# Optimization experiments

Measured on AMD Instinct MI355X. Metric: run time of the kernel, lower is better.

## Reference

```python
import jax, jax.numpy as jnp
import numpy as np

N_NODES = 100000
IN_DIM = 64
OUT_DIM = 64
N_EDGES = 1600000


def setup_inputs() -> dict:
    key = jax.random.key(0)
    k1, k2, k3, k4 = jax.random.split(key, 4)
    x = jax.random.normal(k1, (N_NODES, IN_DIM), dtype=jnp.float32)
    edge_index = jax.random.randint(k2, (2, N_EDGES), 0, N_NODES, dtype=jnp.int32)
    # nn.Linear(in_dim, out_dim): weight [out_dim, in_dim], bias [out_dim]
    bound = 1.0 / np.sqrt(IN_DIM)
    W = jax.random.uniform(k3, (OUT_DIM, IN_DIM), minval=-bound, maxval=bound, dtype=jnp.float32)
    b = jax.random.uniform(k4, (OUT_DIM,), minval=-bound, maxval=bound, dtype=jnp.float32)
    return {"x": x, "edge_index": edge_index, "W": W, "b": b}


def reference(x, edge_index, W, b):
    row, col = edge_index[0], edge_index[1]
    # gather neighbor features and scatter-add into destination rows: [N, in_dim]
    aggr = jax.ops.segment_sum(x[col], row, num_segments=x.shape[0])
    # linear + relu
    return jax.nn.relu(aggr @ W.T + b)
```

## Files before the change

kernel.cpp:

```cpp
#include <hip/hip_runtime.h>
#include <hip/hip_bf16.h>

#define DIM 64
#define BROWS 32
#define BSHIFT 5
#define REGCAP 2048
#define MAXB 4096
#define LCSR_CAP 1024
#define PCHUNK 8192

typedef __attribute__((ext_vector_type(8))) short bf16x8;
typedef __attribute__((ext_vector_type(4))) float f32x4;
typedef __attribute__((ext_vector_type(8))) ushort u16x8;

static __device__ __forceinline__ ushort f2bu(float f) {
  __hip_bfloat16 h = __float2bfloat16(f);
  return *reinterpret_cast<const ushort*>(&h);
}
static __device__ __forceinline__ float bu2f(ushort u) {
  return __uint_as_float(((unsigned)u) << 16);
}

__global__ __launch_bounds__(256) void zero_kernel(int* __restrict__ p, int n) {
  int i = blockIdx.x * 256 + threadIdx.x;
  if (i < n) p[i] = 0;
}

__global__ __launch_bounds__(512) void prep_part_kernel(
    const float* __restrict__ x, const float* __restrict__ W,
    const int* __restrict__ ei, ushort* __restrict__ xb,
    ushort* __restrict__ Wbf, int* __restrict__ bcur, uint* __restrict__ outU,
    int nNodes, int nEdges, int nB, int nPB) {
  __shared__ int h[MAXB];
  __shared__ int base[MAXB];
  const int t = threadIdx.x;

  const int idx = blockIdx.x * 512 + t;
  const int nx8 = nNodes * DIM / 8;
  if (idx < nx8) {
    const f32x4* p = (const f32x4*)(x + (size_t)idx * 8);
    f32x4 v0 = p[0], v1 = p[1];
    u16x8 o;
    o[0] = f2bu(v0[0]); o[1] = f2bu(v0[1]); o[2] = f2bu(v0[2]); o[3] = f2bu(v0[3]);
    o[4] = f2bu(v1[0]); o[5] = f2bu(v1[1]); o[6] = f2bu(v1[2]); o[7] = f2bu(v1[3]);
    *(u16x8*)(xb + (size_t)idx * 8) = o;
  }
  if (blockIdx.x == 0) {
    const int wb = t * 8;
    u16x8 o;
#pragma unroll
    for (int k = 0; k < 8; ++k) o[k] = f2bu(W[wb + k]);
    *(u16x8*)(Wbf + wb) = o;
    if (t < 8) {
      u16x8 z = {0, 0, 0, 0, 0, 0, 0, 0};
      *(u16x8*)(xb + (size_t)nNodes * DIM + t * 8) = z;
    }
  }

  if (blockIdx.x >= nPB) return;

  for (int i = t; i < nB; i += 512) h[i] = 0;
  __syncthreads();
  const int i0 = blockIdx.x * PCHUNK + t * 16;
  int4 r0, r1, r2, r3;
  const bool full = (i0 + 16 <= nEdges);
  if (full) {
    r0 = *(const int4*)(ei + i0);
    r1 = *(const int4*)(ei + i0 + 4);
    r2 = *(const int4*)(ei + i0 + 8);
    r3 = *(const int4*)(ei + i0 + 12);
#define CNT(R) atomicAdd(&h[(R) >> BSHIFT], 1);
    CNT(r0.x) CNT(r0.y) CNT(r0.z) CNT(r0.w)
    CNT(r1.x) CNT(r1.y) CNT(r1.z) CNT(r1.w)
    CNT(r2.x) CNT(r2.y) CNT(r2.z) CNT(r2.w)
    CNT(r3.x) CNT(r3.y) CNT(r3.z) CNT(r3.w)
#undef CNT
  } else if (i0 < nEdges) {
    for (int k = i0; k < nEdges; ++k) atomicAdd(&h[ei[k] >> BSHIFT], 1);
  }
  __syncthreads();
  for (int i = t; i < nB; i += 512) {
    int c = h[i];
    base[i] = c ? atomicAdd(&bcur[i], c) : 0;
  }
  __syncthreads();
  for (int i = t; i < nB; i += 512) h[i] = 0;
  __syncthreads();
#define PUT(RR, CC)                                                       \
  {                                                                       \
    int b_ = (RR) >> BSHIFT;                                              \
    int pos_ = base[b_] + atomicAdd(&h[b_], 1);                           \
    if (pos_ < REGCAP)                                                    \
      outU[(size_t)b_ * REGCAP + pos_] =                                  \
          (((uint)((RR) & (BROWS - 1))) << 27) | (((uint)(CC)) << 7);     \
  }
  if (full) {
    int4 c0 = *(const int4*)(ei + nEdges + i0);
    int4 c1 = *(const int4*)(ei + nEdges + i0 + 4);
    int4 c2 = *(const int4*)(ei + nEdges + i0 + 8);
    int4 c3 = *(const int4*)(ei + nEdges + i0 + 12);
    PUT(r0.x, c0.x) PUT(r0.y, c0.y) PUT(r0.z, c0.z) PUT(r0.w, c0.w)
    PUT(r1.x, c1.x) PUT(r1.y, c1.y) PUT(r1.z, c1.z) PUT(r1.w, c1.w)
    PUT(r2.x, c2.x) PUT(r2.y, c2.y) PUT(r2.z, c2.z) PUT(r2.w, c2.w)
    PUT(r3.x, c3.x) PUT(r3.y, c3.y) PUT(r3.z, c3.z) PUT(r3.w, c3.w)
  } else if (i0 < nEdges) {
    for (int k = i0; k < nEdges; ++k) {
      int row = ei[k], col = ei[nEdges + k];
      PUT(row, col)
    }
  }
#undef PUT
}

__global__ __launch_bounds__(256, 8) void bucket_gather_gemm_kernel(
    const char* __restrict__ xc, float* __restrict__ out,
    const int* __restrict__ bcur, const ushort* __restrict__ Wbf,
    const float* __restrict__ bias, int nNodes) {
  __shared__ int lcsr[LCSR_CAP];
  __shared__ int lhist[BROWS];
  __shared__ int loff[BROWS + 1];
  __shared__ int lcur[BROWS];
  __shared__ ushort sA[BROWS * DIM];

  const int t = threadIdx.x;
  const int bkt = blockIdx.x;
  const int w = t >> 6, lane = t & 63;
  const uint* streamU = (const uint*)(out + (size_t)bkt * REGCAP);
  int cnt = bcur[bkt];
  if (cnt > REGCAP) cnt = REGCAP;

  const bool fast = (cnt + BROWS * 8 <= LCSR_CAP);
  const int rbase = w * 8;

  if (t < BROWS) lhist[t] = 0;
  __syncthreads();

  if (fast) {
    uint p0 = 0, p1 = 0, p2 = 0;
    int nheld = 0;
    {
      int i = t;
      if (i < cnt) { p0 = streamU[i]; nheld = 1; i += 256; }
      if (i < cnt) { p1 = streamU[i]; nheld = 2; i += 256; }
      if (i < cnt) { p2 = streamU[i]; nheld = 3; }
    }
    if (nheld > 0) atomicAdd(&lhist[p0 >> 27], 1);
    if (nheld > 1) atomicAdd(&lhist[p1 >> 27], 1);
    if (nheld > 2) atomicAdd(&lhist[p2 >> 27], 1);
    __syncthreads();
    if (t < BROWS) {
      int d = lhist[t];
      int pd = (d + 7) & ~7;
      if (pd == 0) pd = 8;
      int v = pd;
#pragma unroll
      for (int o = 1; o < BROWS; o <<= 1) {
        int u = __shfl_up(v, o);
        if (t >= o) v += u;
      }
      loff[t] = v - pd;
      lcur[t] = v - pd;
      if (t == BROWS - 1) loff[BROWS] = v;
    }
    __syncthreads();
    if (nheld > 0) { int pos = atomicAdd(&lcur[p0 >> 27], 1); lcsr[pos] = (int)(p0 & 0x07ffffffu); }
    if (nheld > 1) { int pos = atomicAdd(&lcur[p1 >> 27], 1); lcsr[pos] = (int)(p1 & 0x07ffffffu); }
    if (nheld > 2) { int pos = atomicAdd(&lcur[p2 >> 27], 1); lcsr[pos] = (int)(p2 & 0x07ffffffu); }
    __syncthreads();
    if (t < BROWS) {
      int d = lhist[t];
      int pd = (d + 7) & ~7;
      if (pd == 0) pd = 8;
      int o0 = loff[t];
      for (int k = d; k < pd; ++k) lcsr[o0 + k] = nNodes << 7;
    }
    __syncthreads();

    const int half = lane >> 5;
    const int m = lane & 31;
    const char* xlp = xc + (m << 2);

#define ISSUE(v, E)                                   \
    {                                                 \
      int c0_ = lcsr[(E) + 0 + half];                 \
      int c1_ = lcsr[(E) + 2 + half];                 \
      int c2_ = lcsr[(E) + 4 + half];                 \
      int c3_ = lcsr[(E) + 6 + half];                 \
      v##0 = *(const uint*)(xlp + c0_);               \
      v##1 = *(const uint*)(xlp + c1_);               \
      v##2 = *(const uint*)(xlp + c2_);               \
      v##3 = *(const uint*)(xlp + c3_);               \
    }
#define CONSUME(v)                                                          \
    {                                                                       \
      float l01 = __uint_as_float(v##0 << 16) + __uint_as_float(v##1 << 16);\
      float l23 = __uint_as_float(v##2 << 16) + __uint_as_float(v##3 << 16);\
      aLo += l01 + l23;                                                     \
      float h01 = __uint_as_float(v##0 & 0xffff0000u) +                     \
                  __uint_as_float(v##1 & 0xffff0000u);                      \
      float h23 = __uint_as_float(v##2 & 0xffff0000u) +                     \
                  __uint_as_float(v##3 & 0xffff0000u);                      \
      aHi += h01 + h23;                                                     \
    }
#define BOUND                                                               \
    if (e + 8 == rEnd) {                                                    \
      float t0 = aLo + __shfl_xor(aLo, 32);                                 \
      float t1 = aHi + __shfl_xor(aHi, 32);                                 \
      if (lane < 32) {                                                      \
        uint pk = (((uint)f2bu(t1)) << 16) | (uint)f2bu(t0);                \
        int cs = (m >> 2) ^ (r & 7);                                        \
        ((uint*)sA)[r * 32 + cs * 4 + (m & 3)] = pk;                        \
      }                                                                     \
      aLo = 0.f; aHi = 0.f;                                                 \
      ++r;                                                                  \
      rEnd = (r < rbase + 8) ? loff[r + 1] : 0x7fffffff;                    \
    }

    int r = rbase;
    int rEnd = loff[r + 1];
    const int eBeg = loff[rbase];
    const int eEndW = loff[rbase + 8];
    float aLo = 0.f, aHi = 0.f;
    uint vA0, vA1, vA2, vA3, vB0, vB1, vB2, vB3, vC0, vC1, vC2, vC3;

    int e = eBeg;
    ISSUE(vA, e)
    ISSUE(vB, e + 8)
    ISSUE(vC, e + 16)
    for (;;) {
      CONSUME(vA)
      if (e + 24 < eEndW) ISSUE(vA, e + 24)
      BOUND
      e += 8; if (e >= eEndW) break;
      CONSUME(vB)
      if (e + 24 < eEndW) ISSUE(vB, e + 24)
      BOUND
      e += 8; if (e >= eEndW) break;
      CONSUME(vC)
      if (e + 24 < eEndW) ISSUE(vC, e + 24)
      BOUND
      e += 8; if (e >= eEndW) break;
    }
#undef ISSUE
#undef CONSUME
#undef BOUND
  } else {
    for (int rr = 0; rr < 8; ++rr) {
      int r = rbase + rr;
      float acc = 0.f;
      for (int i = 0; i < cnt; ++i) {
        uint p = streamU[i];
        if ((int)(p >> 27) == r)
          acc += bu2f(*(const ushort*)(xc + (p & 0x07ffffffu) + 2 * lane));
      }
      int cs = (lane >> 3) ^ (r & 7);
      sA[r * DIM + cs * 8 + (lane & 7)] = f2bu(acc);
    }
  }

  __syncthreads();

  const int rq = lane & 15, kg = lane >> 4;
  const int h16 = (w & 1) * 16;
  const int ch = w >> 1;
  const int row = h16 + rq;
  const ushort* pr = &sA[row * DIM];
  bf16x8 A0 = *(const bf16x8*)(pr + (((kg) ^ (row & 7)) << 3));
  bf16x8 A1 = *(const bf16x8*)(pr + (((4 + kg) ^ (row & 7)) << 3));

  f32x4 acc4[2] = {f32x4{0, 0, 0, 0}, f32x4{0, 0, 0, 0}};
#pragma unroll
  for (int jt = 0; jt < 2; ++jt) {
    const ushort* bRow = Wbf + (ch * 32 + jt * 16 + rq) * DIM + kg * 8;
    bf16x8 B0 = *(const bf16x8*)(bRow);
    bf16x8 B1 = *(const bf16x8*)(bRow + 32);
    acc4[jt] = __builtin_amdgcn_mfma_f32_16x16x32_bf16(A0, B0, acc4[jt], 0, 0, 0);
    acc4[jt] = __builtin_amdgcn_mfma_f32_16x16x32_bf16(A1, B1, acc4[jt], 0, 0, 0);
  }

  const int nodeBase = bkt * BROWS + h16;
#pragma unroll
  for (int jt = 0; jt < 2; ++jt) {
    int j = ch * 32 + jt * 16 + rq;
    float bj = bias[j];
#pragma unroll
    for (int q = 0; q < 4; ++q) {
      int node = nodeBase + kg * 4 + q;
      out[(size_t)node * DIM + j] = fmaxf(acc4[jt][q] + bj, 0.f);
    }
  }
}

__global__ __launch_bounds__(256) void scatter_add_kernel(
    const float* __restrict__ x, const int* __restrict__ ei,
    float* __restrict__ aggr, int nEdges) {
  const int lane = threadIdx.x & 63;
  const int e = blockIdx.x * 4 + (threadIdx.x >> 6);
  if (e >= nEdges) return;
  const int row = ei[e];
  const int col = ei[nEdges + e];
  atomicAdd(&aggr[(size_t)row * DIM + lane], x[(size_t)col * DIM + lane]);
}

__global__ __launch_bounds__(256) void linear_relu_inplace_kernel(
    float* __restrict__ io, const float* __restrict__ W,
    const float* __restrict__ b, int nRows) {
  __shared__ float sW[64][65];
  __shared__ float sRow[4][64];
  const int tid = threadIdx.x;
  for (int i = tid; i < 64 * 64; i += 256) sW[i >> 6][i & 63] = W[i];
  __syncthreads();
  const int wid = tid >> 6, j = tid & 63;
  const int row = blockIdx.x * 4 + wid;
  if (row < nRows) {
    const size_t base = (size_t)row * DIM;
    sRow[wid][j] = io[base + j];
    float acc = b[j];
#pragma unroll
    for (int k = 0; k < 64; ++k) acc = fmaf(sRow[wid][k], sW[j][k], acc);
    io[base + j] = fmaxf(acc, 0.0f);
  }
}

extern "C" void kernel_launch(void* const* d_in, const int* in_sizes, int n_in,
                              void* d_out, int out_size, void* d_ws, size_t ws_size,
                              hipStream_t stream) {
  const float* x = (const float*)d_in[0];
  const int* ei  = (const int*)d_in[1];
  const float* W = (const float*)d_in[2];
  const float* b = (const float*)d_in[3];
  float* out     = (float*)d_out;

  const int nNodes = in_sizes[0] / DIM;
  const int nEdges = in_sizes[1] / 2;
  const int nB = (nNodes + BROWS - 1) >> BSHIFT;

  size_t off = 0;
  auto take = [&](size_t bytes) {
    size_t r = off;
    off += (bytes + 255) & ~(size_t)255;
    return r;
  };
  char* ws = (char*)d_ws;
  int* bcur   = (int*)(ws + take(MAXB * 4));
  ushort* Wbf = (ushort*)(ws + take(DIM * DIM * 2));
  ushort* xb  = (ushort*)(ws + take((size_t)(nNodes + 1) * DIM * 2));

  const bool fastPath =
      (nNodes < (1 << 20)) && ((nNodes & (BROWS - 1)) == 0) &&
      ((nNodes * DIM) % 8 == 0) &&
      (nB <= MAXB) && (ws_size >= off) &&
      (out_size == nNodes * DIM);

  if (fastPath) {
    const int nPB = (nEdges + PCHUNK - 1) / PCHUNK;
    const int nPrep = (nNodes * DIM / 8 + 511) / 512;
    const int grid = (nPrep > nPB) ? nPrep : nPB;
    zero_kernel<<<(nB + 255) / 256, 256, 0, stream>>>(bcur, nB);
    prep_part_kernel<<<grid, 512, 0, stream>>>(x, W, ei, xb, Wbf, bcur,
                                               (uint*)out, nNodes, nEdges, nB, nPB);
    bucket_gather_gemm_kernel<<<nB, 256, 0, stream>>>(
        (const char*)xb, out, bcur, Wbf, b, nNodes);
  } else {
    hipMemsetAsync(d_out, 0, (size_t)out_size * sizeof(float), stream);
    scatter_add_kernel<<<(nEdges + 3) / 4, 256, 0, stream>>>(x, ei, out, nEdges);
    linear_relu_inplace_kernel<<<(nNodes + 3) / 4, 256, 0, stream>>>(out, W, b, nNodes);
  }
}
```

Before: 67.65 us.

## Gather bf16 rows with 8-byte loads across four edges per wave and pad to 4

The gather loop now has each 16-lane quarter of a wave load one edge's bf16 row as 8-byte uint2 loads, so four edges are handled per step instead of 4-byte loads over two halves. Per-row padding drops from multiples of 8 to multiples of 4, which cuts wasted dummy gathers, and the prefetch depth becomes six in-flight slots of four edges. The fast path also accepts up to 4 stream entries per thread. In exchange the per-row reduction needs two cross-lane shuffle rounds over four accumulators, and the load count per thread changes.

```diff
diff --git a/kernel.cpp b/kernel.cpp
--- a/kernel.cpp
+++ b/kernel.cpp
@@ -129,29 +129,31 @@
   int cnt = bcur[bkt];
   if (cnt > REGCAP) cnt = REGCAP;
 
-  const bool fast = (cnt + BROWS * 8 <= LCSR_CAP);
+  const bool fast = (cnt + BROWS * 4 <= LCSR_CAP);
   const int rbase = w * 8;
 
   if (t < BROWS) lhist[t] = 0;
   __syncthreads();
 
   if (fast) {
-    uint p0 = 0, p1 = 0, p2 = 0;
+    uint p0 = 0, p1 = 0, p2 = 0, p3 = 0;
     int nheld = 0;
     {
       int i = t;
       if (i < cnt) { p0 = streamU[i]; nheld = 1; i += 256; }
       if (i < cnt) { p1 = streamU[i]; nheld = 2; i += 256; }
-      if (i < cnt) { p2 = streamU[i]; nheld = 3; }
+      if (i < cnt) { p2 = streamU[i]; nheld = 3; i += 256; }
+      if (i < cnt) { p3 = streamU[i]; nheld = 4; }
     }
     if (nheld > 0) atomicAdd(&lhist[p0 >> 27], 1);
     if (nheld > 1) atomicAdd(&lhist[p1 >> 27], 1);
     if (nheld > 2) atomicAdd(&lhist[p2 >> 27], 1);
+    if (nheld > 3) atomicAdd(&lhist[p3 >> 27], 1);
     __syncthreads();
     if (t < BROWS) {
       int d = lhist[t];
-      int pd = (d + 7) & ~7;
-      if (pd == 0) pd = 8;
+      int pd = (d + 3) & ~3;
+      if (pd == 0) pd = 4;
       int v = pd;
 #pragma unroll
       for (int o = 1; o < BROWS; o <<= 1) {
@@ -166,52 +168,48 @@
     if (nheld > 0) { int pos = atomicAdd(&lcur[p0 >> 27], 1); lcsr[pos] = (int)(p0 & 0x07ffffffu); }
     if (nheld > 1) { int pos = atomicAdd(&lcur[p1 >> 27], 1); lcsr[pos] = (int)(p1 & 0x07ffffffu); }
     if (nheld > 2) { int pos = atomicAdd(&lcur[p2 >> 27], 1); lcsr[pos] = (int)(p2 & 0x07ffffffu); }
+    if (nheld > 3) { int pos = atomicAdd(&lcur[p3 >> 27], 1); lcsr[pos] = (int)(p3 & 0x07ffffffu); }
     __syncthreads();
     if (t < BROWS) {
       int d = lhist[t];
-      int pd = (d + 7) & ~7;
-      if (pd == 0) pd = 8;
+      int pd = (d + 3) & ~3;
+      if (pd == 0) pd = 4;
       int o0 = loff[t];
       for (int k = d; k < pd; ++k) lcsr[o0 + k] = nNodes << 7;
     }
     __syncthreads();
 
-    const int half = lane >> 5;
-    const int m = lane & 31;
-    const char* xlp = xc + (m << 2);
+    const int q = lane >> 4;
+    const int m = lane & 15;
+    const char* xlp = xc + (m << 3);
 
 #define ISSUE(v, E)                                   \
     {                                                 \
-      int c0_ = lcsr[(E) + 0 + half];                 \
-      int c1_ = lcsr[(E) + 2 + half];                 \
-      int c2_ = lcsr[(E) + 4 + half];                 \
-      int c3_ = lcsr[(E) + 6 + half];                 \
-      v##0 = *(const uint*)(xlp + c0_);               \
-      v##1 = *(const uint*)(xlp + c1_);               \
-      v##2 = *(const uint*)(xlp + c2_);               \
-      v##3 = *(const uint*)(xlp + c3_);               \
-    }
-#define CONSUME(v)                                                          \
-    {                                                                       \
-      float l01 = __uint_as_float(v##0 << 16) + __uint_as_float(v##1 << 16);\
-      float l23 = __uint_as_float(v##2 << 16) + __uint_as_float(v##3 << 16);\
-      aLo += l01 + l23;                                                     \
-      float h01 = __uint_as_float(v##0 & 0xffff0000u) +                     \
-                  __uint_as_float(v##1 & 0xffff0000u);                      \
-      float h23 = __uint_as_float(v##2 & 0xffff0000u) +                     \
-                  __uint_as_float(v##3 & 0xffff0000u);                      \
-      aHi += h01 + h23;                                                     \
+      int c_ = lcsr[(E) + q];                         \
+      v = *(const uint2*)(xlp + c_);                  \
+    }
+#define CONSUME(v)                                    \
+    {                                                 \
+      d0 += __uint_as_float(v.x << 16);               \
+      d1 += __uint_as_float(v.x & 0xffff0000u);       \
+      d2 += __uint_as_float(v.y << 16);               \
+      d3 += __uint_as_float(v.y & 0xffff0000u);       \
     }
 #define BOUND                                                               \
-    if (e + 8 == rEnd) {                                                    \
-      float t0 = aLo + __shfl_xor(aLo, 32);                                 \
-      float t1 = aHi + __shfl_xor(aHi, 32);                                 \
-      if (lane < 32) {                                                      \
-        uint pk = (((uint)f2bu(t1)) << 16) | (uint)f2bu(t0);                \
-        int cs = (m >> 2) ^ (r & 7);                                        \
-        ((uint*)sA)[r * 32 + cs * 4 + (m & 3)] = pk;                        \
+    if (e + 4 == rEnd) {                                                    \
+      d0 += __shfl_xor(d0, 16); d0 += __shfl_xor(d0, 32);                   \
+      d1 += __shfl_xor(d1, 16); d1 += __shfl_xor(d1, 32);                   \
+      d2 += __shfl_xor(d2, 16); d2 += __shfl_xor(d2, 32);                   \
+      d3 += __shfl_xor(d3, 16); d3 += __shfl_xor(d3, 32);                   \
+      if (lane < 16) {                                                      \
+        uint lo = (((uint)f2bu(d1)) << 16) | (uint)f2bu(d0);                \
+        uint hi = (((uint)f2bu(d3)) << 16) | (uint)f2bu(d2);                \
+        int cs = (m >> 1) ^ (r & 7);                                        \
+        uint2* dst = (uint2*)(sA + r * DIM + cs * 8 + (m & 1) * 4);         \
+        uint2 pk; pk.x = lo; pk.y = hi;                                     \
+        *dst = pk;                                                          \
       }                                                                     \
-      aLo = 0.f; aHi = 0.f;                                                 \
+      d0 = 0.f; d1 = 0.f; d2 = 0.f; d3 = 0.f;                               \
       ++r;                                                                  \
       rEnd = (r < rbase + 8) ? loff[r + 1] : 0x7fffffff;                    \
     }
@@ -220,26 +218,41 @@
     int rEnd = loff[r + 1];
     const int eBeg = loff[rbase];
     const int eEndW = loff[rbase + 8];
-    float aLo = 0.f, aHi = 0.f;
-    uint vA0, vA1, vA2, vA3, vB0, vB1, vB2, vB3, vC0, vC1, vC2, vC3;
+    float d0 = 0.f, d1 = 0.f, d2 = 0.f, d3 = 0.f;
+    uint2 v0, v1, v2, v3, v4, v5;
 
     int e = eBeg;
-    ISSUE(vA, e)
-    ISSUE(vB, e + 8)
-    ISSUE(vC, e + 16)
+    ISSUE(v0, e)
+    ISSUE(v1, e + 4)
+    ISSUE(v2, e + 8)
+    ISSUE(v3, e + 12)
+    ISSUE(v4, e + 16)
+    ISSUE(v5, e + 20)
     for (;;) {
-      CONSUME(vA)
-      if (e + 24 < eEndW) ISSUE(vA, e + 24)
-      BOUND
-      e += 8; if (e >= eEndW) break;
-      CONSUME(vB)
-      if (e + 24 < eEndW) ISSUE(vB, e + 24)
-      BOUND
-      e += 8; if (e >= eEndW) break;
-      CONSUME(vC)
-      if (e + 24 < eEndW) ISSUE(vC, e + 24)
-      BOUND
-      e += 8; if (e >= eEndW) break;
+      CONSUME(v0)
+      if (e + 24 < eEndW) ISSUE(v0, e + 24)
+      BOUND
+      e += 4; if (e >= eEndW) break;
+      CONSUME(v1)
+      if (e + 24 < eEndW) ISSUE(v1, e + 24)
+      BOUND
+      e += 4; if (e >= eEndW) break;
+      CONSUME(v2)
+      if (e + 24 < eEndW) ISSUE(v2, e + 24)
+      BOUND
+      e += 4; if (e >= eEndW) break;
+      CONSUME(v3)
+      if (e + 24 < eEndW) ISSUE(v3, e + 24)
+      BOUND
+      e += 4; if (e >= eEndW) break;
+      CONSUME(v4)
+      if (e + 24 < eEndW) ISSUE(v4, e + 24)
+      BOUND
+      e += 4; if (e >= eEndW) break;
+      CONSUME(v5)
+      if (e + 24 < eEndW) ISSUE(v5, e + 24)
+      BOUND
+      e += 4; if (e >= eEndW) break;
     }
 #undef ISSUE
 #undef CONSUME
@@ -284,9 +297,9 @@
     int j = ch * 32 + jt * 16 + rq;
     float bj = bias[j];
 #pragma unroll
-    for (int q = 0; q < 4; ++q) {
-      int node = nodeBase + kg * 4 + q;
-      out[(size_t)node * DIM + j] = fmaxf(acc4[jt][q] + bj, 0.f);
+    for (int qq = 0; qq < 4; ++qq) {
+      int node = nodeBase + kg * 4 + qq;
+      out[(size_t)node * DIM + j] = fmaxf(acc4[jt][qq] + bj, 0.f);
     }
   }
 }
```

After: 70.00 us. 1.03x slower.
